# Performance work log

Measured on AMD Instinct MI355X. Metric: run time of the kernel, lower is better.

## Reference

```python
import jax, jax.numpy as jnp
import numpy as np

N_NODES = 50000
HEADS = 8
NEG_SLOPE = 0.2


def _gat_conv(x, W, a_src, a_dst, b, src, dst, n_nodes):
    """PyG GATConv forward, concat=False (mean over heads), self-loops already in (src, dst)."""
    H, C = a_src.shape
    xl = (x @ W).reshape(n_nodes, H, C)                      # [N, H, C]
    alpha_src = jnp.einsum('nhc,hc->nh', xl, a_src)          # [N, H]
    alpha_dst = jnp.einsum('nhc,hc->nh', xl, a_dst)          # [N, H]
    alpha = jax.nn.leaky_relu(alpha_src[src] + alpha_dst[dst], NEG_SLOPE)  # [E, H]
    # segment softmax over edges grouped by destination node
    amax = jax.ops.segment_max(alpha, dst, num_segments=n_nodes)           # [N, H]
    amax = jnp.where(jnp.isfinite(amax), amax, jnp.zeros_like(amax))
    ex = jnp.exp(alpha - jax.lax.stop_gradient(amax)[dst])                  # [E, H]
    denom = jax.ops.segment_sum(ex, dst, num_segments=n_nodes)             # [N, H]
    coef = ex / (denom[dst] + 1e-16)                                        # [E, H]
    msg = xl[src] * coef[:, :, None]                                        # [E, H, C]
    out = jax.ops.segment_sum(msg, dst, num_segments=n_nodes)              # [N, H, C]
    return out.mean(axis=1) + b                                             # [N, C]


def setup_inputs() -> dict:
    key = jax.random.key(0)
    ks = jax.random.split(key, 12)
    in_feats, h_feats, out_feats = 256, 64, 64
    n_edges = 800000
    x = jax.random.normal(ks[0], (N_NODES, in_feats), dtype=jnp.float32)
    edge_index = jax.random.randint(ks[1], (2, n_edges), 0, N_NODES, dtype=jnp.int64)
    # Glorot-ish init for weights
    def glorot(k, shape, fan):
        return jax.random.normal(k, shape, dtype=jnp.float32) * (1.0 / np.sqrt(fan))
    W1 = glorot(ks[2], (in_feats, HEADS * h_feats), in_feats)
    a_src1 = glorot(ks[3], (HEADS, h_feats), h_feats)
    a_dst1 = glorot(ks[4], (HEADS, h_feats), h_feats)
    b1 = jnp.zeros((h_feats,), dtype=jnp.float32)
    W2 = glorot(ks[5], (h_feats, HEADS * out_feats), h_feats)
    a_src2 = glorot(ks[6], (HEADS, out_feats), out_feats)
    a_dst2 = glorot(ks[7], (HEADS, out_feats), out_feats)
    b2 = jnp.zeros((out_feats,), dtype=jnp.float32)
    return {"x": x, "edge_index": edge_index,
            "W1": W1, "a_src1": a_src1, "a_dst1": a_dst1, "b1": b1,
            "W2": W2, "a_src2": a_src2, "a_dst2": a_dst2, "b2": b2}


def reference(x, edge_index, W1, a_src1, a_dst1, b1, W2, a_src2, a_dst2, b2):
    n = x.shape[0]
    # PyG GATConv add_self_loops=True (default): append self loops
    loops = jnp.arange(n, dtype=edge_index.dtype)
    src = jnp.concatenate([edge_index[0], loops])
    dst = jnp.concatenate([edge_index[1], loops])
    # F.dropout(p=0.6) is identity in eval mode
    h = _gat_conv(x, W1, a_src1, a_dst1, b1, src, dst, n)
    h = jax.nn.relu(h)
    out = _gat_conv(h, W2, a_src2, a_dst2, b2, src, dst, n)
    return out
```

## Files before the change

### kernel.cpp

```cpp
#include <hip/hip_runtime.h>

#define NN 50000
#define MPAD 50048
#define HD 8
#define CD 64
#define NHF 512
#define SCAN_B 256
#define NBLK ((NN + SCAN_B - 1) / SCAN_B)

typedef __attribute__((ext_vector_type(8))) short short8v;
typedef __attribute__((ext_vector_type(8))) unsigned short us8;
typedef __attribute__((ext_vector_type(4))) unsigned short us4;
typedef __attribute__((ext_vector_type(4))) float f32x4;
typedef __attribute__((ext_vector_type(8))) _Float16 h8;

__device__ inline unsigned short f32_to_bf16(float f) {
    unsigned int u = __float_as_uint(f);
    unsigned int r = (u + 0x7fffu + ((u >> 16) & 1u)) >> 16;
    return (unsigned short)r;
}
__device__ inline float bf16_to_f32(unsigned short h) {
    return __uint_as_float(((unsigned int)h) << 16);
}

__global__ void k_init_cnt(int* __restrict__ cnt) {
    int i = blockIdx.x * 256 + threadIdx.x;
    if (i < NN) cnt[i] = 1;
}

__global__ void k_hist(const int* __restrict__ dst, int E, int* __restrict__ cnt) {
    int e = blockIdx.x * 256 + threadIdx.x;
    if (e < E) atomicAdd(&cnt[dst[e]], 1);
}

__global__ __launch_bounds__(SCAN_B) void k_block_sums(const int* __restrict__ cnt,
                                                       int* __restrict__ bsums) {
    __shared__ int sdata[4];
    int i = blockIdx.x * SCAN_B + threadIdx.x;
    int v = (i < NN) ? cnt[i] : 0;
#pragma unroll
    for (int off = 1; off < 64; off <<= 1) v += __shfl_xor(v, off);
    if ((threadIdx.x & 63) == 0) sdata[threadIdx.x >> 6] = v;
    __syncthreads();
    if (threadIdx.x == 0) bsums[blockIdx.x] = sdata[0] + sdata[1] + sdata[2] + sdata[3];
}

__global__ __launch_bounds__(SCAN_B) void k_scan_bsums(const int* __restrict__ bsums,
                                                       int* __restrict__ boffs, int nblk) {
    __shared__ int tmp[SCAN_B];
    int tid = threadIdx.x;
    int v = (tid < nblk) ? bsums[tid] : 0;
    tmp[tid] = v;
    __syncthreads();
    for (int off = 1; off < SCAN_B; off <<= 1) {
        int t = (tid >= off) ? tmp[tid - off] : 0;
        __syncthreads();
        tmp[tid] += t;
        __syncthreads();
    }
    if (tid < nblk) boffs[tid] = tmp[tid] - v;
}

__global__ __launch_bounds__(SCAN_B) void k_emit(const int* __restrict__ cnt,
                                                 const int* __restrict__ boffs,
                                                 int* __restrict__ row_ptr,
                                                 int* __restrict__ cursor,
                                                 int* __restrict__ csr_src) {
    __shared__ int tmp[SCAN_B];
    int tid = threadIdx.x;
    int i = blockIdx.x * SCAN_B + tid;
    int v = (i < NN) ? cnt[i] : 0;
    tmp[tid] = v;
    __syncthreads();
    for (int off = 1; off < SCAN_B; off <<= 1) {
        int t = (tid >= off) ? tmp[tid - off] : 0;
        __syncthreads();
        tmp[tid] += t;
        __syncthreads();
    }
    int base = boffs[blockIdx.x] + tmp[tid] - v;
    if (i < NN) {
        row_ptr[i] = base;
        csr_src[base] = i;
        cursor[i] = base + 1;
        if (i == NN - 1) row_ptr[NN] = base + v;
    }
}

__global__ void k_scatter(const int* __restrict__ src, const int* __restrict__ dst,
                          int E, int* __restrict__ cursor, int* __restrict__ csr_src) {
    int e = blockIdx.x * 256 + threadIdx.x;
    if (e < E) {
        int pos = atomicAdd(&cursor[dst[e]], 1);
        csr_src[pos] = src[e];
    }
}

__global__ void k_split_bt(const float* __restrict__ B, unsigned short* __restrict__ bht,
                           unsigned short* __restrict__ blt, int K) {
    int idx = blockIdx.x * 256 + threadIdx.x;
    if (idx < K * NHF) {
        int k = idx >> 9, n = idx & 511;
        float v = B[idx];
        unsigned short hb = f32_to_bf16(v);
        float l = v - bf16_to_f32(hb);
        blt[n * K + k] = f32_to_bf16(l);
        bht[n * K + k] = hb;
    }
}

__global__ void k_split_a(const float* __restrict__ A, unsigned short* __restrict__ ah,
                          unsigned short* __restrict__ al, int M, int K) {
    int idx = blockIdx.x * 256 + threadIdx.x;
    int tot = (MPAD * K) >> 2;
    if (idx >= tot) return;
    int row = (idx << 2) / K;
    float4 v = make_float4(0.f, 0.f, 0.f, 0.f);
    if (row < M) v = *(const float4*)(A + ((size_t)idx << 2));
    us4 hs, ls;
    hs.x = f32_to_bf16(v.x); ls.x = f32_to_bf16(v.x - bf16_to_f32(hs.x));
    hs.y = f32_to_bf16(v.y); ls.y = f32_to_bf16(v.y - bf16_to_f32(hs.y));
    hs.z = f32_to_bf16(v.z); ls.z = f32_to_bf16(v.z - bf16_to_f32(hs.z));
    hs.w = f32_to_bf16(v.w); ls.w = f32_to_bf16(v.w - bf16_to_f32(hs.w));
    *(us4*)(ah + ((size_t)idx << 2)) = hs;
    *(us4*)(al + ((size_t)idx << 2)) = ls;
}

#define BM 128
#define BN 128
#define BKF 32
#define LDK 40

__global__ __launch_bounds__(256) void k_gemm_mfma(
    const unsigned short* __restrict__ Aht,
    const unsigned short* __restrict__ Alt,
    const unsigned short* __restrict__ Bht,
    const unsigned short* __restrict__ Blt,
    const float* __restrict__ a_src, const float* __restrict__ a_dst,
    _Float16* __restrict__ C, float* __restrict__ asrc_out, float* __restrict__ adst_out,
    int M, int K)
{
    __shared__ unsigned short Ash[BM][LDK];
    __shared__ unsigned short Asl[BM][LDK];
    __shared__ unsigned short Bsh[BN][LDK];
    __shared__ unsigned short Bsl[BN][LDK];

    const int t = threadIdx.x;
    const int lane = t & 63;
    const int wid = t >> 6;
    const int wr = wid >> 1, wc = wid & 1;
    const int bm = blockIdx.x * BM;
    const int bn = blockIdx.y * BN;
    const int l15 = lane & 15;
    const int lg = lane >> 4;

    f32x4 acc[4][4];
#pragma unroll
    for (int mi = 0; mi < 4; ++mi)
#pragma unroll
        for (int ni = 0; ni < 4; ++ni)
            acc[mi][ni] = (f32x4){0.f, 0.f, 0.f, 0.f};

    const int srow = t >> 1;
    const int skc = (t & 1) * 16;

    for (int k0 = 0; k0 < K; k0 += BKF) {
        __syncthreads();
        {
            const unsigned short* gah = Aht + (size_t)(bm + srow) * K + k0 + skc;
            const unsigned short* gal = Alt + (size_t)(bm + srow) * K + k0 + skc;
            const unsigned short* gbh = Bht + (size_t)(bn + srow) * K + k0 + skc;
            const unsigned short* gbl = Blt + (size_t)(bn + srow) * K + k0 + skc;
            *(us8*)&Ash[srow][skc]     = *(const us8*)gah;
            *(us8*)&Ash[srow][skc + 8] = *(const us8*)(gah + 8);
            *(us8*)&Asl[srow][skc]     = *(const us8*)gal;
            *(us8*)&Asl[srow][skc + 8] = *(const us8*)(gal + 8);
            *(us8*)&Bsh[srow][skc]     = *(const us8*)gbh;
            *(us8*)&Bsh[srow][skc + 8] = *(const us8*)(gbh + 8);
            *(us8*)&Bsl[srow][skc]     = *(const us8*)gbl;
            *(us8*)&Bsl[srow][skc + 8] = *(const us8*)(gbl + 8);
        }
        __syncthreads();

        short8v ah[4], al[4], bh[4], bl[4];
#pragma unroll
        for (int i = 0; i < 4; ++i) {
            ah[i] = *(const short8v*)&Ash[wr * 64 + i * 16 + l15][lg * 8];
            al[i] = *(const short8v*)&Asl[wr * 64 + i * 16 + l15][lg * 8];
            bh[i] = *(const short8v*)&Bsh[wc * 64 + i * 16 + l15][lg * 8];
            bl[i] = *(const short8v*)&Bsl[wc * 64 + i * 16 + l15][lg * 8];
        }
#pragma unroll
        for (int mi = 0; mi < 4; ++mi)
#pragma unroll
            for (int ni = 0; ni < 4; ++ni) {
                acc[mi][ni] = __builtin_amdgcn_mfma_f32_16x16x32_bf16(ah[mi], bh[ni], acc[mi][ni], 0, 0, 0);
                acc[mi][ni] = __builtin_amdgcn_mfma_f32_16x16x32_bf16(ah[mi], bl[ni], acc[mi][ni], 0, 0, 0);
                acc[mi][ni] = __builtin_amdgcn_mfma_f32_16x16x32_bf16(al[mi], bh[ni], acc[mi][ni], 0, 0, 0);
            }
    }

    const int head_w = (bn >> 6) + wc;
    float ca[4], cd[4];
#pragma unroll
    for (int ni = 0; ni < 4; ++ni) {
        ca[ni] = a_src[head_w * 64 + ni * 16 + l15];
        cd[ni] = a_dst[head_w * 64 + ni * 16 + l15];
    }
#pragma unroll
    for (int mi = 0; mi < 4; ++mi) {
#pragma unroll
        for (int r = 0; r < 4; ++r) {
            int row = bm + wr * 64 + mi * 16 + lg * 4 + r;
            float ps = 0.f, pd = 0.f;
#pragma unroll
            for (int ni = 0; ni < 4; ++ni) {
                float cv = acc[mi][ni][r];
                int col = bn + wc * 64 + ni * 16 + l15;
                if (row < M) C[(size_t)row * NHF + col] = (_Float16)cv;
                ps += cv * ca[ni];
                pd += cv * cd[ni];
            }
#pragma unroll
            for (int off = 1; off < 16; off <<= 1) {
                ps += __shfl_xor(ps, off);
                pd += __shfl_xor(pd, off);
            }
            if (l15 == 0 && row < M) {
                asrc_out[row * HD + head_w] = ps;
                adst_out[row * HD + head_w] = pd;
            }
        }
    }
}

__global__ __launch_bounds__(256) void k_aggregate(
    const _Float16* __restrict__ xl, const float* __restrict__ asrc,
    const float* __restrict__ adst, const int* __restrict__ row_ptr,
    const int* __restrict__ csr_src, const float* __restrict__ bias,
    float* __restrict__ out, unsigned short* __restrict__ o_hi,
    unsigned short* __restrict__ o_lo, int mode)
{
    __shared__ float sh[4][NHF];
    const int wid  = threadIdx.x >> 6;
    const int lane = threadIdx.x & 63;
    const int n    = blockIdx.x * 4 + wid;
    const int head = lane >> 3;
    const int off  = lane * 8;

    const float ad = adst[n * HD + head];
    const int e0 = row_ptr[n];
    const int e1 = row_ptr[n + 1];

    float acc[8] = {};
    float s = 0.f;

    int e = e0;
    for (; e + 4 <= e1; e += 4) {
        int i0 = csr_src[e];
        int i1 = csr_src[e + 1];
        int i2 = csr_src[e + 2];
        int i3 = csr_src[e + 3];
        float a0 = asrc[i0 * HD + head];
        float a1 = asrc[i1 * HD + head];
        float a2 = asrc[i2 * HD + head];
        float a3 = asrc[i3 * HD + head];
        h8 v0 = *(const h8*)(xl + (size_t)i0 * NHF + off);
        h8 v1 = *(const h8*)(xl + (size_t)i1 * NHF + off);
        h8 v2 = *(const h8*)(xl + (size_t)i2 * NHF + off);
        h8 v3 = *(const h8*)(xl + (size_t)i3 * NHF + off);
        a0 += ad; a1 += ad; a2 += ad; a3 += ad;
        float p0 = __expf(a0 > 0.f ? a0 : 0.2f * a0);
        float p1 = __expf(a1 > 0.f ? a1 : 0.2f * a1);
        float p2 = __expf(a2 > 0.f ? a2 : 0.2f * a2);
        float p3 = __expf(a3 > 0.f ? a3 : 0.2f * a3);
        s += p0 + p1 + p2 + p3;
#pragma unroll
        for (int j = 0; j < 8; ++j) {
            acc[j] += p0 * (float)v0[j];
            acc[j] += p1 * (float)v1[j];
            acc[j] += p2 * (float)v2[j];
            acc[j] += p3 * (float)v3[j];
        }
    }
    for (; e < e1; ++e) {
        int i0 = csr_src[e];
        float a = asrc[i0 * HD + head] + ad;
        h8 vv = *(const h8*)(xl + (size_t)i0 * NHF + off);
        float p = __expf(a > 0.f ? a : 0.2f * a);
        s += p;
#pragma unroll
        for (int j = 0; j < 8; ++j) acc[j] += p * (float)vv[j];
    }

    const float inv = 1.f / (s + 1e-16f);
#pragma unroll
    for (int j = 0; j < 8; ++j) sh[wid][off + j] = acc[j] * inv;
    __syncthreads();

    float sum = 0.f;
#pragma unroll
    for (int h2 = 0; h2 < HD; ++h2) sum += sh[wid][h2 * CD + lane];
    float res = sum * 0.125f + bias[lane];
    if (mode) {
        res = fmaxf(res, 0.f);
        unsigned short hb = f32_to_bf16(res);
        o_hi[(size_t)n * CD + lane] = hb;
        o_lo[(size_t)n * CD + lane] = f32_to_bf16(res - bf16_to_f32(hb));
    } else {
        out[(size_t)n * CD + lane] = res;
    }
}

extern "C" void kernel_launch(void* const* d_in, const int* in_sizes, int n_in,
                              void* d_out, int out_size, void* d_ws, size_t ws_size,
                              hipStream_t stream) {
    const float* x   = (const float*)d_in[0];
    const int*   ei  = (const int*)d_in[1];
    const float* W1  = (const float*)d_in[2];
    const float* as1 = (const float*)d_in[3];
    const float* ad1 = (const float*)d_in[4];
    const float* b1  = (const float*)d_in[5];
    const float* W2  = (const float*)d_in[6];
    const float* as2 = (const float*)d_in[7];
    const float* ad2 = (const float*)d_in[8];
    const float* b2  = (const float*)d_in[9];

    const int E = in_sizes[1] / 2;
    const int* esrc = ei;
    const int* edst = ei + E;

    char* ws = (char*)d_ws;
    _Float16* xlh        = (_Float16*)ws;
    unsigned short* Ah1  = (unsigned short*)(ws + 51200000);
    unsigned short* Al1  = (unsigned short*)(ws + 76824576);
    float* asrc          = (float*)(ws + 102449152);
    float* adst          = (float*)(ws + 104049152);
    unsigned short* Hh   = (unsigned short*)(ws + 105649152);
    unsigned short* Hl   = (unsigned short*)(ws + 112055296);
    int*   row_ptr       = (int*)(ws + 118461440);
    int*   cursor        = (int*)(ws + 118661632);
    int*   csr_src       = (int*)(ws + 118861632);
    unsigned short* Bht1 = (unsigned short*)(ws + 122261632);
    unsigned short* Blt1 = (unsigned short*)(ws + 122523776);
    unsigned short* Bht2 = (unsigned short*)(ws + 122785920);
    unsigned short* Blt2 = (unsigned short*)(ws + 122851456);
    int*   bsums         = (int*)(ws + 122916992);
    int*   boffs         = (int*)(ws + 122917888);

    k_init_cnt<<<(NN + 255) / 256, 256, 0, stream>>>(cursor);
    k_hist<<<(E + 255) / 256, 256, 0, stream>>>(edst, E, cursor);
    k_block_sums<<<NBLK, SCAN_B, 0, stream>>>(cursor, bsums);
    k_scan_bsums<<<1, SCAN_B, 0, stream>>>(bsums, boffs, NBLK);
    k_emit<<<NBLK, SCAN_B, 0, stream>>>(cursor, boffs, row_ptr, cursor, csr_src);
    k_scatter<<<(E + 255) / 256, 256, 0, stream>>>(esrc, edst, E, cursor, csr_src);

    k_split_bt<<<(256 * NHF + 255) / 256, 256, 0, stream>>>(W1, Bht1, Blt1, 256);
    k_split_bt<<<(64 * NHF + 255) / 256, 256, 0, stream>>>(W2, Bht2, Blt2, 64);
    k_split_a<<<((MPAD * 256 / 4) + 255) / 256, 256, 0, stream>>>(x, Ah1, Al1, NN, 256);

    dim3 gemm_grid(MPAD / BM, NHF / BN);

    k_gemm_mfma<<<gemm_grid, 256, 0, stream>>>(Ah1, Al1, Bht1, Blt1, as1, ad1,
                                               xlh, asrc, adst, NN, 256);
    k_aggregate<<<NN / 4, 256, 0, stream>>>(xlh, asrc, adst, row_ptr, csr_src, b1,
                                            nullptr, Hh, Hl, 1);

    k_gemm_mfma<<<gemm_grid, 256, 0, stream>>>(Hh, Hl, Bht2, Blt2, as2, ad2,
                                               xlh, asrc, adst, NN, 64);
    k_aggregate<<<NN / 4, 256, 0, stream>>>(xlh, asrc, adst, row_ptr, csr_src, b2,
                                            (float*)d_out, nullptr, nullptr, 0);
}
```

Baseline: 482.7 us.

## Fuse fp32-to-bf16 split of x into GEMM and widen tile to 256 columns

Drops the separate kernel that split x into bf16 hi/lo arrays. The first GEMM now loads fp32 x directly and does the hi/lo conversion while staging into shared memory. The GEMM block also grows to 512 threads with a 128x256 output tile, so each A tile is reused across more columns. This saves a full write and read of the split A arrays, but the epilogue has to be consistent with the new 4-column-wave layout, and the larger block may reduce occupancy.

After: 452.0 us. -6.4%, faster.

```diff
diff --git a/kernel.cpp b/kernel.cpp
--- a/kernel.cpp
+++ b/kernel.cpp
@@ -109,29 +109,14 @@
     }
 }
 
-__global__ void k_split_a(const float* __restrict__ A, unsigned short* __restrict__ ah,
-                          unsigned short* __restrict__ al, int M, int K) {
-    int idx = blockIdx.x * 256 + threadIdx.x;
-    int tot = (MPAD * K) >> 2;
-    if (idx >= tot) return;
-    int row = (idx << 2) / K;
-    float4 v = make_float4(0.f, 0.f, 0.f, 0.f);
-    if (row < M) v = *(const float4*)(A + ((size_t)idx << 2));
-    us4 hs, ls;
-    hs.x = f32_to_bf16(v.x); ls.x = f32_to_bf16(v.x - bf16_to_f32(hs.x));
-    hs.y = f32_to_bf16(v.y); ls.y = f32_to_bf16(v.y - bf16_to_f32(hs.y));
-    hs.z = f32_to_bf16(v.z); ls.z = f32_to_bf16(v.z - bf16_to_f32(hs.z));
-    hs.w = f32_to_bf16(v.w); ls.w = f32_to_bf16(v.w - bf16_to_f32(hs.w));
-    *(us4*)(ah + ((size_t)idx << 2)) = hs;
-    *(us4*)(al + ((size_t)idx << 2)) = ls;
-}
-
 #define BM 128
-#define BN 128
+#define BN 256
 #define BKF 32
 #define LDK 40
 
-__global__ __launch_bounds__(256) void k_gemm_mfma(
+template<int SPLIT>
+__global__ __launch_bounds__(512) void k_gemm(
+    const float* __restrict__ Af,
     const unsigned short* __restrict__ Aht,
     const unsigned short* __restrict__ Alt,
     const unsigned short* __restrict__ Bht,
@@ -148,7 +133,8 @@
     const int t = threadIdx.x;
     const int lane = t & 63;
     const int wid = t >> 6;
-    const int wr = wid >> 1, wc = wid & 1;
+    const int wr = wid >> 2;
+    const int wc = wid & 3;
     const int bm = blockIdx.x * BM;
     const int bn = blockIdx.y * BN;
     const int l15 = lane & 15;
@@ -161,24 +147,52 @@
         for (int ni = 0; ni < 4; ++ni)
             acc[mi][ni] = (f32x4){0.f, 0.f, 0.f, 0.f};
 
-    const int srow = t >> 1;
-    const int skc = (t & 1) * 16;
+    const int srowA = t >> 2;
+    const int skcA  = (t & 3) * 8;
+    const int srowB = t >> 1;
+    const int skcB  = (t & 1) * 16;
 
     for (int k0 = 0; k0 < K; k0 += BKF) {
         __syncthreads();
+        if (SPLIT) {
+            const int gr = bm + srowA;
+            if (gr < M) {
+                const float* ga = Af + (size_t)gr * K + k0 + skcA;
+                float4 v0 = *(const float4*)ga;
+                float4 v1 = *(const float4*)(ga + 4);
+                us4 h0, l0, h1, l1;
+                h0.x = f32_to_bf16(v0.x); l0.x = f32_to_bf16(v0.x - bf16_to_f32(h0.x));
+                h0.y = f32_to_bf16(v0.y); l0.y = f32_to_bf16(v0.y - bf16_to_f32(h0.y));
+                h0.z = f32_to_bf16(v0.z); l0.z = f32_to_bf16(v0.z - bf16_to_f32(h0.z));
+                h0.w = f32_to_bf16(v0.w); l0.w = f32_to_bf16(v0.w - bf16_to_f32(h0.w));
+                h1.x = f32_to_bf16(v1.x); l1.x = f32_to_bf16(v1.x - bf16_to_f32(h1.x));
+                h1.y = f32_to_bf16(v1.y); l1.y = f32_to_bf16(v1.y - bf16_to_f32(h1.y));
+                h1.z = f32_to_bf16(v1.z); l1.z = f32_to_bf16(v1.z - bf16_to_f32(h1.z));
+                h1.w = f32_to_bf16(v1.w); l1.w = f32_to_bf16(v1.w - bf16_to_f32(h1.w));
+                *(us4*)&Ash[srowA][skcA]     = h0;
+                *(us4*)&Ash[srowA][skcA + 4] = h1;
+                *(us4*)&Asl[srowA][skcA]     = l0;
+                *(us4*)&Asl[srowA][skcA + 4] = l1;
+            } else {
+                us4 z = (us4){0, 0, 0, 0};
+                *(us4*)&Ash[srowA][skcA]     = z;
+                *(us4*)&Ash[srowA][skcA + 4] = z;
+                *(us4*)&Asl[srowA][skcA]     = z;
+                *(us4*)&Asl[srowA][skcA + 4] = z;
+            }
+        } else {
+            const unsigned short* gah = Aht + (size_t)(bm + srowA) * K + k0 + skcA;
+            const unsigned short* gal = Alt + (size_t)(bm + srowA) * K + k0 + skcA;
+            *(us8*)&Ash[srowA][skcA] = *(const us8*)gah;
+            *(us8*)&Asl[srowA][skcA] = *(const us8*)gal;
+        }
         {
-            const unsigned short* gah = Aht + (size_t)(bm + srow) * K + k0 + skc;
-            const unsigned short* gal = Alt + (size_t)(bm + srow) * K + k0 + skc;
-            const unsigned short* gbh = Bht + (size_t)(bn + srow) * K + k0 + skc;
-            const unsigned short* gbl = Blt + (size_t)(bn + srow) * K + k0 + skc;
-            *(us8*)&Ash[srow][skc]     = *(const us8*)gah;
-            *(us8*)&Ash[srow][skc + 8] = *(const us8*)(gah + 8);
-            *(us8*)&Asl[srow][skc]     = *(const us8*)gal;
-            *(us8*)&Asl[srow][skc + 8] = *(const us8*)(gal + 8);
-            *(us8*)&Bsh[srow][skc]     = *(const us8*)gbh;
-            *(us8*)&Bsh[srow][skc + 8] = *(const us8*)(gbh + 8);
-            *(us8*)&Bsl[srow][skc]     = *(const us8*)gbl;
-            *(us8*)&Bsl[srow][skc + 8] = *(const us8*)(gbl + 8);
+            const unsigned short* gbh = Bht + (size_t)(bn + srowB) * K + k0 + skcB;
+            const unsigned short* gbl = Blt + (size_t)(bn + srowB) * K + k0 + skcB;
+            *(us8*)&Bsh[srowB][skcB]     = *(const us8*)gbh;
+            *(us8*)&Bsh[srowB][skcB + 8] = *(const us8*)(gbh + 8);
+            *(us8*)&Bsl[srowB][skcB]     = *(const us8*)gbl;
+            *(us8*)&Bsl[srowB][skcB + 8] = *(const us8*)(gbl + 8);
         }
         __syncthreads();
 
@@ -332,21 +346,19 @@
 
     char* ws = (char*)d_ws;
     _Float16* xlh        = (_Float16*)ws;
-    unsigned short* Ah1  = (unsigned short*)(ws + 51200000);
-    unsigned short* Al1  = (unsigned short*)(ws + 76824576);
-    float* asrc          = (float*)(ws + 102449152);
-    float* adst          = (float*)(ws + 104049152);
-    unsigned short* Hh   = (unsigned short*)(ws + 105649152);
-    unsigned short* Hl   = (unsigned short*)(ws + 112055296);
-    int*   row_ptr       = (int*)(ws + 118461440);
-    int*   cursor        = (int*)(ws + 118661632);
-    int*   csr_src       = (int*)(ws + 118861632);
-    unsigned short* Bht1 = (unsigned short*)(ws + 122261632);
-    unsigned short* Blt1 = (unsigned short*)(ws + 122523776);
-    unsigned short* Bht2 = (unsigned short*)(ws + 122785920);
-    unsigned short* Blt2 = (unsigned short*)(ws + 122851456);
-    int*   bsums         = (int*)(ws + 122916992);
-    int*   boffs         = (int*)(ws + 122917888);
+    float* asrc          = (float*)(ws + 51200000);
+    float* adst          = (float*)(ws + 52800000);
+    unsigned short* Hh   = (unsigned short*)(ws + 54400000);
+    unsigned short* Hl   = (unsigned short*)(ws + 60806144);
+    int*   row_ptr       = (int*)(ws + 67212288);
+    int*   cursor        = (int*)(ws + 67412480);
+    int*   csr_src       = (int*)(ws + 67612480);
+    unsigned short* Bht1 = (unsigned short*)(ws + 71012480);
+    unsigned short* Blt1 = (unsigned short*)(ws + 71274624);
+    unsigned short* Bht2 = (unsigned short*)(ws + 71536768);
+    unsigned short* Blt2 = (unsigned short*)(ws + 71602304);
+    int*   bsums         = (int*)(ws + 71667840);
+    int*   boffs         = (int*)(ws + 71668736);
 
     k_init_cnt<<<(NN + 255) / 256, 256, 0, stream>>>(cursor);
     k_hist<<<(E + 255) / 256, 256, 0, stream>>>(edst, E, cursor);
@@ -357,17 +369,16 @@
 
     k_split_bt<<<(256 * NHF + 255) / 256, 256, 0, stream>>>(W1, Bht1, Blt1, 256);
     k_split_bt<<<(64 * NHF + 255) / 256, 256, 0, stream>>>(W2, Bht2, Blt2, 64);
-    k_split_a<<<((MPAD * 256 / 4) + 255) / 256, 256, 0, stream>>>(x, Ah1, Al1, NN, 256);
 
     dim3 gemm_grid(MPAD / BM, NHF / BN);
 
-    k_gemm_mfma<<<gemm_grid, 256, 0, stream>>>(Ah1, Al1, Bht1, Blt1, as1, ad1,
-                                               xlh, asrc, adst, NN, 256);
+    k_gemm<1><<<gemm_grid, 512, 0, stream>>>(x, nullptr, nullptr, Bht1, Blt1, as1, ad1,
+                                             xlh, asrc, adst, NN, 256);
     k_aggregate<<<NN / 4, 256, 0, stream>>>(xlh, asrc, adst, row_ptr, csr_src, b1,
                                             nullptr, Hh, Hl, 1);
 
-    k_gemm_mfma<<<gemm_grid, 256, 0, stream>>>(Hh, Hl, Bht2, Blt2, as2, ad2,
-                                               xlh, asrc, adst, NN, 64);
+    k_gemm<0><<<gemm_grid, 512, 0, stream>>>(nullptr, Hh, Hl, Bht2, Blt2, as2, ad2,
+                                             xlh, asrc, adst, NN, 64);
     k_aggregate<<<NN / 4, 256, 0, stream>>>(xlh, asrc, adst, row_ptr, csr_src, b2,
                                             (float*)d_out, nullptr, nullptr, 0);
 }
```
